# Optimization experiments

Measured on AMD Instinct MI355X. Metric: run time of the kernel, lower is better.

Reference implementation:

```python
import jax, jax.numpy as jnp
import numpy as np

B, L_IN, T = 1024, 512, 96
IN_DIM, OUT_DIM = 1, 1
H_ENC, H_DEC = 128, 256  # decoder hidden = 2 * encoder hidden (bidir concat)


def _lstm_cell(x, h, c, Wih, Whh, b):
    # PyTorch gate order: i, f, g, o. b = b_ih + b_hh (equivalent to two biases).
    gates = x @ Wih.T + h @ Whh.T + b
    i, f, g, o = jnp.split(gates, 4, axis=-1)
    c = jax.nn.sigmoid(f) * c + jax.nn.sigmoid(i) * jnp.tanh(g)
    h = jax.nn.sigmoid(o) * jnp.tanh(c)
    return h, c


def _lstm_final(xs, Wih, Whh, b, hidden, reverse=False):
    # xs: [L, B, D]; returns final (h, c) only (encoder outputs are unused).
    h0 = jnp.zeros((xs.shape[1], hidden), xs.dtype)
    c0 = jnp.zeros((xs.shape[1], hidden), xs.dtype)

    def step(carry, x):
        h, c = _lstm_cell(x, carry[0], carry[1], Wih, Whh, b)
        return (h, c), None

    (h, c), _ = jax.lax.scan(step, (h0, c0), xs, reverse=reverse)
    return h, c


def setup_inputs() -> dict:
    key = jax.random.key(0)
    ks = jax.random.split(key, 13)
    p = lambda k, s: (jax.random.normal(k, s, jnp.float32) * 0.05)
    return {
        "source": jax.random.normal(ks[0], (B, L_IN, IN_DIM), jnp.float32),
        "target_tensor": jnp.zeros((B, T, OUT_DIM), jnp.float32),
        "enc_Wih_f": p(ks[1], (4 * H_ENC, IN_DIM)),
        "enc_Whh_f": p(ks[2], (4 * H_ENC, H_ENC)),
        "enc_b_f": p(ks[3], (4 * H_ENC,)),
        "enc_Wih_b": p(ks[4], (4 * H_ENC, IN_DIM)),
        "enc_Whh_b": p(ks[5], (4 * H_ENC, H_ENC)),
        "enc_b_b": p(ks[6], (4 * H_ENC,)),
        "dec_Wih": p(ks[7], (4 * H_DEC, OUT_DIM)),
        "dec_Whh": p(ks[8], (4 * H_DEC, H_DEC)),
        "dec_b": p(ks[9], (4 * H_DEC,)),
        "out_W": p(ks[10], (OUT_DIM, H_DEC)),
        "out_b": p(ks[11], (OUT_DIM,)),
    }


def reference(source, target_tensor, enc_Wih_f, enc_Whh_f, enc_b_f,
              enc_Wih_b, enc_Whh_b, enc_b_b,
              dec_Wih, dec_Whh, dec_b, out_W, out_b):
    batch = source.shape[0]
    t_len = target_tensor.shape[1]
    out_dim = target_tensor.shape[-1]

    xs = jnp.swapaxes(source, 0, 1)  # [L, B, IN]
    h_f, c_f = _lstm_final(xs, enc_Wih_f, enc_Whh_f, enc_b_f, H_ENC, reverse=False)
    h_b, c_b = _lstm_final(xs, enc_Wih_b, enc_Whh_b, enc_b_b, H_ENC, reverse=True)
    h0 = jnp.concatenate([h_f, h_b], axis=-1)  # [B, 2*H_ENC]
    c0 = jnp.concatenate([c_f, c_b], axis=-1)

    y0 = jnp.zeros((batch, out_dim), source.dtype)

    def dec_step(carry, _):
        h, c, y = carry
        h, c = _lstm_cell(y, h, c, dec_Wih, dec_Whh, dec_b)
        y = h @ out_W.T + out_b
        return (h, c, y), y

    _, ys = jax.lax.scan(dec_step, (h0, c0, y0), None, length=t_len)
    return jnp.swapaxes(ys, 0, 1)  # [B, T, OUT]
```

## Files before the change

kernel.cpp:

```cpp
#include <hip/hip_runtime.h>
#include <math.h>

#define H_ENC 128
#define H_DEC 256
#define L_SRC 512
#define T_DEC 96
#define B_TOT 1024

typedef _Float16 half8 __attribute__((ext_vector_type(8)));
typedef float f32x4 __attribute__((ext_vector_type(4)));

#define MFMA16(A, B, C) __builtin_amdgcn_mfma_f32_16x16x32_f16((A), (B), (C), 0, 0, 0)

__device__ __forceinline__ unsigned packu(float a, float b) {
    union { _Float16 h[2]; unsigned u; } x; x.h[0] = (_Float16)a; x.h[1] = (_Float16)b; return x.u;
}

__device__ __forceinline__ float sigmoidf_(float x) {
    return __builtin_amdgcn_rcpf(1.f + __expf(-x));
}
__device__ __forceinline__ float tanhf_(float x) {
    return 1.f - 2.f * __builtin_amdgcn_rcpf(__expf(2.f * x) + 1.f);
}

#define CNT_STRIDE 104
__global__ void zero_cnt(int* cnt) {
    int i = blockIdx.x * blockDim.x + threadIdx.x;
    if (i < 64 * CNT_STRIDE) cnt[i] = 0;
}

#define EB 8
#define HPAD 136
__global__ __launch_bounds__(1024)
void encoder_big(
    const float* __restrict__ source,
    const float* __restrict__ Wih_f, const float* __restrict__ Whh_f, const float* __restrict__ b_f,
    const float* __restrict__ Wih_b, const float* __restrict__ Whh_b, const float* __restrict__ b_b,
    float* __restrict__ h0, float* __restrict__ c0)
{
    const int dir = blockIdx.x & 1;
    const int bg  = blockIdx.x >> 1;
    const int t   = threadIdx.x;
    const int w   = t >> 6;
    const int l   = t & 63;
    const int col = l & 15;
    const int grp = l >> 4;

    const float* Wih = dir ? Wih_b : Wih_f;
    const float* Whh = dir ? Whh_b : Whh_f;
    const float* bb  = dir ? b_b   : b_f;

    __shared__ float    xsT[L_SRC][EB];
    __shared__ _Float16 hbuf[2][16][HPAD];
    __shared__ float    gbuf[4][EB][H_ENC];

    {
        const float* srcb = source + (size_t)bg * EB * L_SRC;
        for (int i = t; i < EB * L_SRC; i += 1024) {
            int b = i >> 9, st = i & 511;
            xsT[st][b] = srcb[i];
        }
        for (int i = t; i < 2 * 16 * HPAD; i += 1024)
            ((_Float16*)hbuf)[i] = (_Float16)0.f;
    }

    half8 wf[2][4];
    #pragma unroll
    for (int tau = 0; tau < 2; ++tau) {
        const int n = 2 * w + tau;
        const int grow = (n >> 3) * H_ENC + 16 * (n & 7) + col;
        const float* wr = Whh + (size_t)grow * H_ENC;
        #pragma unroll
        for (int kt = 0; kt < 4; ++kt) {
            const float* p = wr + 32 * kt + 8 * grp;
            float4 v0 = *reinterpret_cast<const float4*>(p);
            float4 v1 = *reinterpret_cast<const float4*>(p + 4);
            half8 h;
            h[0] = (_Float16)v0.x; h[1] = (_Float16)v0.y; h[2] = (_Float16)v0.z; h[3] = (_Float16)v0.w;
            h[4] = (_Float16)v1.x; h[5] = (_Float16)v1.y; h[6] = (_Float16)v1.z; h[7] = (_Float16)v1.w;
            wf[tau][kt] = h;
        }
    }

    const int ub = t >> 7;
    const int ue = t & 127;
    const float bI = bb[ue],           wI = Wih[ue];
    const float bF = bb[H_ENC + ue],   wF = Wih[H_ENC + ue];
    const float bG = bb[2*H_ENC + ue], wG = Wih[2*H_ENC + ue];
    const float bO = bb[3*H_ENC + ue], wO = Wih[3*H_ENC + ue];

    float c = 0.f, hlast = 0.f;
    __syncthreads();

    int cur = 0;
    for (int s = 0; s < L_SRC; ++s) {
        const int step = dir ? (L_SRC - 1 - s) : s;

        half8 a0 = *reinterpret_cast<const half8*>(&hbuf[cur][col][ 0 + 8 * grp]);
        half8 a1 = *reinterpret_cast<const half8*>(&hbuf[cur][col][32 + 8 * grp]);
        half8 a2 = *reinterpret_cast<const half8*>(&hbuf[cur][col][64 + 8 * grp]);
        half8 a3 = *reinterpret_cast<const half8*>(&hbuf[cur][col][96 + 8 * grp]);

        f32x4 acc0 = {0.f, 0.f, 0.f, 0.f};
        f32x4 acc1 = {0.f, 0.f, 0.f, 0.f};
        acc0 = MFMA16(a0, wf[0][0], acc0); acc0 = MFMA16(a1, wf[0][1], acc0);
        acc0 = MFMA16(a2, wf[0][2], acc0); acc0 = MFMA16(a3, wf[0][3], acc0);
        acc1 = MFMA16(a0, wf[1][0], acc1); acc1 = MFMA16(a1, wf[1][1], acc1);
        acc1 = MFMA16(a2, wf[1][2], acc1); acc1 = MFMA16(a3, wf[1][3], acc1);

        if (grp < 2) {
            #pragma unroll
            for (int tau = 0; tau < 2; ++tau) {
                const int n = 2 * w + tau;
                const int G = n >> 3;
                const int e = 16 * (n & 7) + col;
                const f32x4 acc = tau ? acc1 : acc0;
                #pragma unroll
                for (int r = 0; r < 4; ++r)
                    gbuf[G][4 * grp + r][e] = acc[r];
            }
        }
        __syncthreads();

        {
            float x = xsT[step][ub];
            float gi = sigmoidf_(gbuf[0][ub][ue] + bI + wI * x);
            float gf = sigmoidf_(gbuf[1][ub][ue] + bF + wF * x);
            float gg = tanhf_  (gbuf[2][ub][ue] + bG + wG * x);
            float go = sigmoidf_(gbuf[3][ub][ue] + bO + wO * x);
            c = gf * c + gi * gg;
            float h = go * tanhf_(c);
            hlast = h;
            hbuf[cur ^ 1][ub][ue] = (_Float16)h;
        }
        __syncthreads();
        cur ^= 1;
    }

    h0[(size_t)(bg * EB + ub) * (2 * H_ENC) + dir * H_ENC + ue] = hlast;
    c0[(size_t)(bg * EB + ub) * (2 * H_ENC) + dir * H_ENC + ue] = c;
}

#define DB 16
__global__ __launch_bounds__(512, 2)
void decoder_split(
    const float* __restrict__ Wih,
    const float* __restrict__ bb,
    const float* __restrict__ outW,
    const float* __restrict__ outb,
    const float* __restrict__ h0,
    const float* __restrict__ c0,
    const float* __restrict__ Whh,
    unsigned* __restrict__ hx,
    int* __restrict__ cnt,
    float* __restrict__ out)
{
    const int blk = blockIdx.x;
    const int bg  = blk & 63;
    const int q   = blk >> 6;
    const int t   = threadIdx.x;
    const int w   = t >> 6;
    const int l   = t & 63;
    const int col = l & 15;
    const int grp = l >> 4;
    const int u   = w >> 1;
    const int fo  = w & 1;

    __shared__ unsigned hlU[DB][132];
    __shared__ float    exch[4][2][DB][16];
    __shared__ unsigned hnewU[DB][32];
    __shared__ float    yl[DB];
    __shared__ float    owl[H_DEC];
    int* mycnt = cnt + bg * CNT_STRIDE;

    if (t < H_DEC) owl[t] = outW[t];

    const int j0 = 64 * q + 16 * u + col;
    const int rA = (fo ? 256 : 0) + j0;
    const int rB = (fo ? 768 : 512) + j0;

    half8 wfA[8], wfB[8];
    #pragma unroll
    for (int kt = 0; kt < 8; ++kt) {
        const float* pa = Whh + (size_t)rA * H_DEC + 32 * kt + 8 * grp;
        const float* pb = Whh + (size_t)rB * H_DEC + 32 * kt + 8 * grp;
        float4 a0 = *reinterpret_cast<const float4*>(pa);
        float4 a1 = *reinterpret_cast<const float4*>(pa + 4);
        float4 b0 = *reinterpret_cast<const float4*>(pb);
        float4 b1 = *reinterpret_cast<const float4*>(pb + 4);
        half8 ha, hb;
        ha[0]=(_Float16)a0.x; ha[1]=(_Float16)a0.y; ha[2]=(_Float16)a0.z; ha[3]=(_Float16)a0.w;
        ha[4]=(_Float16)a1.x; ha[5]=(_Float16)a1.y; ha[6]=(_Float16)a1.z; ha[7]=(_Float16)a1.w;
        hb[0]=(_Float16)b0.x; hb[1]=(_Float16)b0.y; hb[2]=(_Float16)b0.z; hb[3]=(_Float16)b0.w;
        hb[4]=(_Float16)b1.x; hb[5]=(_Float16)b1.y; hb[6]=(_Float16)b1.z; hb[7]=(_Float16)b1.w;
        wfA[kt] = ha; wfB[kt] = hb;
    }

    const float bI = bb[j0],       wI = Wih[j0];
    const float bF = bb[256 + j0], wF = Wih[256 + j0];
    const float bG = bb[512 + j0], wG = Wih[512 + j0];
    const float bO = bb[768 + j0], wO = Wih[768 + j0];
    const float ob = outb[0];

    float c[4];
    #pragma unroll
    for (int r = 0; r < 4; ++r)
        c[r] = c0[(size_t)(bg * DB + 4 * grp + r) * H_DEC + j0];

    {
        int batch = t >> 5, pair = t & 31;
        int e = 64 * q + 2 * pair;
        const float* hp = h0 + (size_t)(bg * DB + batch) * H_DEC + e;
        unsigned v = packu(hp[0], hp[1]);
        __hip_atomic_store(&hx[(size_t)(bg * DB + batch) * 128 + 32 * q + pair], v,
                           __ATOMIC_RELAXED, __HIP_MEMORY_SCOPE_AGENT);
    }
    __syncthreads();
    if (t == 0) {
        __hip_atomic_fetch_add(&mycnt[0], 1, __ATOMIC_RELEASE, __HIP_MEMORY_SCOPE_AGENT);
        while (__hip_atomic_load(&mycnt[0], __ATOMIC_RELAXED, __HIP_MEMORY_SCOPE_AGENT) < 4) {}
    }
    __syncthreads();

    for (int s = 1; s <= T_DEC; ++s) {
        const int rb = (s - 1) & 1, wb = s & 1;
        #pragma unroll
        for (int i = 0; i < 4; ++i) {
            int j = t + 512 * i;
            int batch = j >> 7, within = j & 127;
            unsigned v = __hip_atomic_load(
                &hx[(size_t)rb * (B_TOT * 128) + (size_t)(bg * DB + batch) * 128 + within],
                __ATOMIC_RELAXED, __HIP_MEMORY_SCOPE_AGENT);
            hlU[batch][within] = v;
        }
        __syncthreads();

        {
            int batch = t >> 5, seg = t & 31;
            half8 hv = *reinterpret_cast<const half8*>(
                reinterpret_cast<const char*>(hlU) + batch * 528 + seg * 16);
            float sum = 0.f;
            #pragma unroll
            for (int j = 0; j < 8; ++j) sum += (float)hv[j] * owl[8 * seg + j];
            #pragma unroll
            for (int m = 1; m < 32; m <<= 1) sum += __shfl_xor(sum, m);
            if (seg == 0) {
                float yv = sum + ob;
                yl[batch] = (s == 1) ? 0.f : yv;
                if (q == 0 && s >= 2) out[(size_t)(bg * DB + batch) * T_DEC + (s - 2)] = yv;
            }
        }

        half8 a[8];
        #pragma unroll
        for (int kt = 0; kt < 8; ++kt)
            a[kt] = *reinterpret_cast<const half8*>(
                reinterpret_cast<const char*>(hlU) + col * 528 + (32 * kt + 8 * grp) * 2);

        f32x4 accA = {0.f, 0.f, 0.f, 0.f};
        f32x4 accB = {0.f, 0.f, 0.f, 0.f};
        #pragma unroll
        for (int kt = 0; kt < 8; ++kt) {
            accA = MFMA16(a[kt], wfA[kt], accA);
            accB = MFMA16(a[kt], wfB[kt], accB);
        }

        if (fo) {
            #pragma unroll
            for (int r = 0; r < 4; ++r) {
                exch[u][0][4 * grp + r][col] = accA[r] + bF;
                exch[u][1][4 * grp + r][col] = accB[r] + bO;
            }
        }
        __syncthreads();

        if (!fo) {
            #pragma unroll
            for (int r = 0; r < 4; ++r) {
                float yb = yl[4 * grp + r];
                float gi = sigmoidf_(accA[r] + bI + wI * yb);
                float gg = tanhf_  (accB[r] + bG + wG * yb);
                float gf = sigmoidf_(exch[u][0][4 * grp + r][col] + wF * yb);
                float go = sigmoidf_(exch[u][1][4 * grp + r][col] + wO * yb);
                c[r] = gf * c[r] + gi * gg;
                float h = go * tanhf_(c[r]);
                reinterpret_cast<_Float16*>(hnewU)[(4 * grp + r) * 64 + 16 * u + col] = (_Float16)h;
            }
        }
        __syncthreads();

        {
            int batch = t >> 5, pair = t & 31;
            __hip_atomic_store(
                &hx[(size_t)wb * (B_TOT * 128) + (size_t)(bg * DB + batch) * 128 + 32 * q + pair],
                hnewU[batch][pair], __ATOMIC_RELAXED, __HIP_MEMORY_SCOPE_AGENT);
        }
        __syncthreads();
        if (t == 0) {
            __hip_atomic_fetch_add(&mycnt[s], 1, __ATOMIC_RELEASE, __HIP_MEMORY_SCOPE_AGENT);
            while (__hip_atomic_load(&mycnt[s], __ATOMIC_RELAXED, __HIP_MEMORY_SCOPE_AGENT) < 4) {}
        }
        __syncthreads();
    }

    {
        #pragma unroll
        for (int i = 0; i < 4; ++i) {
            int j = t + 512 * i;
            int batch = j >> 7, within = j & 127;
            unsigned v = __hip_atomic_load(
                &hx[(size_t)(bg * DB + batch) * 128 + within],
                __ATOMIC_RELAXED, __HIP_MEMORY_SCOPE_AGENT);
            hlU[batch][within] = v;
        }
        __syncthreads();
        int batch = t >> 5, seg = t & 31;
        half8 hv = *reinterpret_cast<const half8*>(
            reinterpret_cast<const char*>(hlU) + batch * 528 + seg * 16);
        float sum = 0.f;
        #pragma unroll
        for (int j = 0; j < 8; ++j) sum += (float)hv[j] * owl[8 * seg + j];
        #pragma unroll
        for (int m = 1; m < 32; m <<= 1) sum += __shfl_xor(sum, m);
        if (q == 0 && seg == 0)
            out[(size_t)(bg * DB + batch) * T_DEC + (T_DEC - 1)] = sum + ob;
    }
}

extern "C" void kernel_launch(void* const* d_in, const int* in_sizes, int n_in,
                              void* d_out, int out_size, void* d_ws, size_t ws_size,
                              hipStream_t stream) {
    const float* source = (const float*)d_in[0];
    const float* eWih_f = (const float*)d_in[2];
    const float* eWhh_f = (const float*)d_in[3];
    const float* eb_f   = (const float*)d_in[4];
    const float* eWih_b = (const float*)d_in[5];
    const float* eWhh_b = (const float*)d_in[6];
    const float* eb_b   = (const float*)d_in[7];
    const float* dWih   = (const float*)d_in[8];
    const float* dWhh   = (const float*)d_in[9];
    const float* db     = (const float*)d_in[10];
    const float* oW     = (const float*)d_in[11];
    const float* obp    = (const float*)d_in[12];
    float* out = (float*)d_out;

    float*    h0  = (float*)d_ws;
    float*    c0  = h0 + (size_t)B_TOT * H_DEC;
    unsigned* hx  = (unsigned*)(c0 + (size_t)B_TOT * H_DEC);
    int*      cnt = (int*)(hx + (size_t)2 * B_TOT * 128);

    zero_cnt<<<(64 * CNT_STRIDE + 255) / 256, 256, 0, stream>>>(cnt);
    encoder_big<<<128 * 2, 1024, 0, stream>>>(
        source, eWih_f, eWhh_f, eb_f, eWih_b, eWhh_b, eb_b, h0, c0);
    decoder_split<<<256, 512, 0, stream>>>(
        dWih, db, oW, obp, h0, c0, dWhh, hx, cnt, out);
}
```

Baseline: 915.0 us.

## Halve encoder batch tile to four rows and relax decoder barrier atomics

```diff
diff --git a/kernel.cpp b/kernel.cpp
--- a/kernel.cpp
+++ b/kernel.cpp
@@ -29,10 +29,10 @@
     if (i < 64 * CNT_STRIDE) cnt[i] = 0;
 }
 
-#define EB 8
+#define EB 4
 #define HPAD 136
-__global__ __launch_bounds__(1024)
-void encoder_big(
+__global__ __launch_bounds__(512, 4)
+void encoder_eb4r(
     const float* __restrict__ source,
     const float* __restrict__ Wih_f, const float* __restrict__ Whh_f, const float* __restrict__ b_f,
     const float* __restrict__ Wih_b, const float* __restrict__ Whh_b, const float* __restrict__ b_b,
@@ -51,23 +51,23 @@
     const float* bb  = dir ? b_b   : b_f;
 
     __shared__ float    xsT[L_SRC][EB];
-    __shared__ _Float16 hbuf[2][16][HPAD];
+    __shared__ _Float16 hbuf[2][EB][HPAD];
     __shared__ float    gbuf[4][EB][H_ENC];
 
     {
         const float* srcb = source + (size_t)bg * EB * L_SRC;
-        for (int i = t; i < EB * L_SRC; i += 1024) {
+        for (int i = t; i < EB * L_SRC; i += 512) {
             int b = i >> 9, st = i & 511;
             xsT[st][b] = srcb[i];
         }
-        for (int i = t; i < 2 * 16 * HPAD; i += 1024)
+        for (int i = t; i < 2 * EB * HPAD; i += 512)
             ((_Float16*)hbuf)[i] = (_Float16)0.f;
     }
 
-    half8 wf[2][4];
+    half8 wf[4][4];
     #pragma unroll
-    for (int tau = 0; tau < 2; ++tau) {
-        const int n = 2 * w + tau;
+    for (int tau = 0; tau < 4; ++tau) {
+        const int n = 4 * w + tau;
         const int grow = (n >> 3) * H_ENC + 16 * (n & 7) + col;
         const float* wr = Whh + (size_t)grow * H_ENC;
         #pragma unroll
@@ -96,28 +96,37 @@
     for (int s = 0; s < L_SRC; ++s) {
         const int step = dir ? (L_SRC - 1 - s) : s;
 
-        half8 a0 = *reinterpret_cast<const half8*>(&hbuf[cur][col][ 0 + 8 * grp]);
-        half8 a1 = *reinterpret_cast<const half8*>(&hbuf[cur][col][32 + 8 * grp]);
-        half8 a2 = *reinterpret_cast<const half8*>(&hbuf[cur][col][64 + 8 * grp]);
-        half8 a3 = *reinterpret_cast<const half8*>(&hbuf[cur][col][96 + 8 * grp]);
+        half8 a0 = {0,0,0,0,0,0,0,0}, a1 = a0, a2 = a0, a3 = a0;
+        if (col < EB) {
+            a0 = *reinterpret_cast<const half8*>(&hbuf[cur][col][ 0 + 8 * grp]);
+            a1 = *reinterpret_cast<const half8*>(&hbuf[cur][col][32 + 8 * grp]);
+            a2 = *reinterpret_cast<const half8*>(&hbuf[cur][col][64 + 8 * grp]);
+            a3 = *reinterpret_cast<const half8*>(&hbuf[cur][col][96 + 8 * grp]);
+        }
 
         f32x4 acc0 = {0.f, 0.f, 0.f, 0.f};
         f32x4 acc1 = {0.f, 0.f, 0.f, 0.f};
+        f32x4 acc2 = {0.f, 0.f, 0.f, 0.f};
+        f32x4 acc3 = {0.f, 0.f, 0.f, 0.f};
         acc0 = MFMA16(a0, wf[0][0], acc0); acc0 = MFMA16(a1, wf[0][1], acc0);
         acc0 = MFMA16(a2, wf[0][2], acc0); acc0 = MFMA16(a3, wf[0][3], acc0);
         acc1 = MFMA16(a0, wf[1][0], acc1); acc1 = MFMA16(a1, wf[1][1], acc1);
         acc1 = MFMA16(a2, wf[1][2], acc1); acc1 = MFMA16(a3, wf[1][3], acc1);
-
-        if (grp < 2) {
-            #pragma unroll
-            for (int tau = 0; tau < 2; ++tau) {
-                const int n = 2 * w + tau;
+        acc2 = MFMA16(a0, wf[2][0], acc2); acc2 = MFMA16(a1, wf[2][1], acc2);
+        acc2 = MFMA16(a2, wf[2][2], acc2); acc2 = MFMA16(a3, wf[2][3], acc2);
+        acc3 = MFMA16(a0, wf[3][0], acc3); acc3 = MFMA16(a1, wf[3][1], acc3);
+        acc3 = MFMA16(a2, wf[3][2], acc3); acc3 = MFMA16(a3, wf[3][3], acc3);
+
+        if (grp == 0) {
+            #pragma unroll
+            for (int tau = 0; tau < 4; ++tau) {
+                const int n = 4 * w + tau;
                 const int G = n >> 3;
                 const int e = 16 * (n & 7) + col;
-                const f32x4 acc = tau ? acc1 : acc0;
+                const f32x4 acc = (tau == 0) ? acc0 : (tau == 1) ? acc1 : (tau == 2) ? acc2 : acc3;
                 #pragma unroll
                 for (int r = 0; r < 4; ++r)
-                    gbuf[G][4 * grp + r][e] = acc[r];
+                    gbuf[G][r][e] = acc[r];
             }
         }
         __syncthreads();
@@ -217,8 +226,9 @@
     }
     __syncthreads();
     if (t == 0) {
-        __hip_atomic_fetch_add(&mycnt[0], 1, __ATOMIC_RELEASE, __HIP_MEMORY_SCOPE_AGENT);
-        while (__hip_atomic_load(&mycnt[0], __ATOMIC_RELAXED, __HIP_MEMORY_SCOPE_AGENT) < 4) {}
+        __hip_atomic_fetch_add(&mycnt[0], 1, __ATOMIC_RELAXED, __HIP_MEMORY_SCOPE_AGENT);
+        while (__hip_atomic_load(&mycnt[0], __ATOMIC_RELAXED, __HIP_MEMORY_SCOPE_AGENT) < 4)
+            __builtin_amdgcn_s_sleep(1);
     }
     __syncthreads();
 
@@ -297,8 +307,9 @@
         }
         __syncthreads();
         if (t == 0) {
-            __hip_atomic_fetch_add(&mycnt[s], 1, __ATOMIC_RELEASE, __HIP_MEMORY_SCOPE_AGENT);
-            while (__hip_atomic_load(&mycnt[s], __ATOMIC_RELAXED, __HIP_MEMORY_SCOPE_AGENT) < 4) {}
+            __hip_atomic_fetch_add(&mycnt[s], 1, __ATOMIC_RELAXED, __HIP_MEMORY_SCOPE_AGENT);
+            while (__hip_atomic_load(&mycnt[s], __ATOMIC_RELAXED, __HIP_MEMORY_SCOPE_AGENT) < 4)
+                __builtin_amdgcn_s_sleep(1);
         }
         __syncthreads();
     }
@@ -350,7 +361,7 @@
     int*      cnt = (int*)(hx + (size_t)2 * B_TOT * 128);
 
     zero_cnt<<<(64 * CNT_STRIDE + 255) / 256, 256, 0, stream>>>(cnt);
-    encoder_big<<<128 * 2, 1024, 0, stream>>>(
+    encoder_eb4r<<<256 * 2, 512, 0, stream>>>(
         source, eWih_f, eWhh_f, eb_f, eWih_b, eWhh_b, eb_b, h0, c0);
     decoder_split<<<256, 512, 0, stream>>>(
         dWih, db, oW, obp, h0, c0, dWhh, hx, cnt, out);
```

Result: faster. 822.6 us (-10.1%).
